# Kernel tuning notes

Hardware: AMD Instinct MI355X
Metric: run time of the kernel (lower is better)

## Reference

```python
import jax, jax.numpy as jnp
import numpy as np


def setup_inputs() -> dict:
    key = jax.random.key(0)
    k1, k2 = jax.random.split(key)
    N, F, E = 100000, 128, 600000
    x = jax.random.normal(k1, (N, F), dtype=jnp.float32)
    edge_index = jax.random.randint(k2, (2, E), 0, N, dtype=jnp.int64)
    return {"x": x, "edge_index": edge_index}


def reference(x, edge_index):
    # x: [N, F] node features; edge_index: [2, E]
    ei = edge_index.T  # [E, 2]
    N = x.shape[0]
    E = ei.shape[0]

    # Midpoint node insertion: mean of the two endpoint features per edge.
    mid = 0.5 * (x[ei[:, 0]] + x[ei[:, 1]])  # [E, F]
    new_x = jnp.concatenate([x, mid], axis=0)  # [N+E, F]

    # New node indices N .. N+E-1
    new_idx = jnp.arange(N, N + E)
    e1 = jnp.stack([ei[:, 0], new_idx], axis=1)  # src -> midpoint
    e2 = jnp.stack([new_idx, ei[:, 1]], axis=1)  # midpoint -> dst

    # Triangle edges among consecutive triples of new nodes (vectorized form
    # of the original Python loop: for i in range(N, N+E-2, 3)).
    T = -(-(E - 2) // 3) if E > 2 else 0  # ceil((E-2)/3) == number of loop iters
    i = N + 3 * jnp.arange(T)
    tri = jnp.stack([i, i + 1, i + 1, i + 2, i + 2, i], axis=1).reshape(-1, 2)  # [3T, 2]

    new_ei = jnp.concatenate([ei, e1, e2, tri], axis=0)  # [E + 2E + 3T, 2]
    return new_x, new_ei.T
```

## Files before the change

### kernel.cpp

```cpp
#include <hip/hip_runtime.h>


#define F 128
#define F4 32
#define BSHIFT 10
#define SLOTS 8192
#define SPB_BLOCKS (SLOTS / 16)
#define CHUNK 2048

typedef float f32x4 __attribute__((ext_vector_type(4)));

__device__ __forceinline__ void nt_store4(f32x4 v, f32x4* p) {
    asm volatile("global_store_dwordx4 %0, %1, off sc0 sc1 nt"
                 :: "v"(p), "v"(v) : "memory");
}
__device__ __forceinline__ void nt_store1(float v, float* p) {
    asm volatile("global_store_dword %0, %1, off sc0 sc1 nt"
                 :: "v"(p), "v"(v) : "memory");
}

__global__ void init_kernel(int4* __restrict__ tup, int* __restrict__ cursor,
                            int NB, int nSlots) {
    const int i = blockIdx.x * blockDim.x + threadIdx.x;
    if (i < nSlots) tup[i] = make_int4(0, 0, -1, 0);
    if (blockIdx.x == 0 && threadIdx.x < NB)
        cursor[threadIdx.x] = threadIdx.x * SLOTS;
}

__global__ __launch_bounds__(256) void scatter_kernel(
        const int* __restrict__ ei0, const int* __restrict__ ei1,
        int* __restrict__ cursor, int4* __restrict__ tup, int E, int NB) {
    __shared__ int lh[128];
    __shared__ int lbase[128];
    const int t = threadIdx.x;
    if (t < 128) lh[t] = 0;
    __syncthreads();
    const int base = blockIdx.x * CHUNK;
    int s[8], d[8], bk[8], rk[8];
#pragma unroll
    for (int i = 0; i < 8; ++i) {
        const int e = base + i * 256 + t;
        if (e < E) {
            s[i] = ei0[e];
            d[i] = ei1[e];
            bk[i] = s[i] >> BSHIFT;
            rk[i] = atomicAdd(&lh[bk[i]], 1);
        } else {
            bk[i] = -1;
        }
    }
    __syncthreads();
    if (t < NB) {
        const int c = lh[t];
        lbase[t] = c ? atomicAdd(&cursor[t], c) : 0;
    }
    __syncthreads();
#pragma unroll
    for (int i = 0; i < 8; ++i) {
        if (bk[i] >= 0) {
            const int e = base + i * 256 + t;
            const int pos = lbase[bk[i]] + rk[i];
            if (pos < (bk[i] + 1) * SLOTS)
                tup[pos] = make_int4(s[i], d[i], e, 0);
        }
    }
}

__global__ __launch_bounds__(256) void main_kernel(
        const f32x4* __restrict__ x4,
        const int* __restrict__ ei0, const int* __restrict__ ei1,
        const int4* __restrict__ tup,
        f32x4* __restrict__ out4, float* __restrict__ r0, float* __restrict__ r1,
        int N, int E, int M, int NB, int MB, int EBlk) {
    const unsigned b = blockIdx.x;

    if (b < (unsigned)MB) {
        const int xcd = b & 7;
        const int seq = b >> 3;
        const int bucket = xcd + 8 * (seq / SPB_BLOCKS);
        if (bucket >= NB) return;
        const int chunk = seq % SPB_BLOCKS;
        const int slot0 = bucket * SLOTS + chunk * 16;
        const int lane = threadIdx.x & 31;
        const int g = threadIdx.x >> 5;
        const int p0 = slot0 + g * 2;

        const int4 t0 = tup[p0];
        const int4 t1 = tup[p0 + 1];
        f32x4 a0 = 0.f, b0v = 0.f, a1 = 0.f, b1v = 0.f;
        if (t0.z >= 0) {
            a0  = x4[t0.x * F4 + lane];
            b0v = x4[t0.y * F4 + lane];
        }
        if (t1.z >= 0) {
            a1  = x4[t1.x * F4 + lane];
            b1v = x4[t1.y * F4 + lane];
        }
        if (t0.z >= 0)
            nt_store4(0.5f * (a0 + b0v), &out4[(size_t)(N + t0.z) * F4 + lane]);
        if (t1.z >= 0)
            nt_store4(0.5f * (a1 + b1v), &out4[(size_t)(N + t1.z) * F4 + lane]);
        return;
    }

    const unsigned eb = b - MB;
    if (eb < (unsigned)EBlk) {
        const int col = eb * 256 + threadIdx.x;
        if (col >= M) return;
        int a, c;
        if (col < E) {
            a = ei0[col];
            c = ei1[col];
        } else if (col < 2 * E) {
            const int e = col - E;
            a = ei0[e];
            c = N + e;
        } else if (col < 3 * E) {
            const int e = col - 2 * E;
            a = N + e;
            c = ei1[e];
        } else {
            const int j = col - 3 * E;
            const int tt = j / 3;
            const int k = j - 3 * tt;
            const int i = N + 3 * tt;
            a = i + k;
            c = (k < 2) ? (i + k + 1) : i;
        }
        nt_store1((float)a, &r0[col]);
        nt_store1((float)c, &r1[col]);
        return;
    }

    const unsigned cb = eb - EBlk;
    const int lane = threadIdx.x & 31;
    const int g = threadIdx.x >> 5;
    const long long row0 = (long long)cb * 16 + g * 2;
    if (row0 < N) {
        f32x4 v0 = x4[row0 * F4 + lane];
        nt_store4(v0, &out4[row0 * F4 + lane]);
    }
    const long long row1 = row0 + 1;
    if (row1 < N) {
        f32x4 v1 = x4[row1 * F4 + lane];
        nt_store4(v1, &out4[row1 * F4 + lane]);
    }
}

extern "C" void kernel_launch(void* const* d_in, const int* in_sizes, int n_in,
                              void* d_out, int out_size, void* d_ws, size_t ws_size,
                              hipStream_t stream) {
    const float* x = (const float*)d_in[0];
    const int* ei = (const int*)d_in[1];

    const int N = in_sizes[0] / F;
    const int E = in_sizes[1] / 2;
    const int T = (E > 2) ? (E - 2 + 2) / 3 : 0;
    const int M = 3 * E + 3 * T;

    const int* ei0 = ei;
    const int* ei1 = ei + E;

    float* out = (float*)d_out;
    float* r0 = out + (size_t)(N + E) * F;
    float* r1 = r0 + M;

    int* cursor = (int*)d_ws;
    int4* tup = (int4*)((char*)d_ws + 4096);

    const int NB = (N + (1 << BSHIFT) - 1) >> BSHIFT;
    const int NBpad = (NB + 7) & ~7;
    const int nSlots = NB * SLOTS;
    const int MB = NBpad * SPB_BLOCKS;
    const int EBlk = (M + 255) / 256;
    const int CB = (N + 15) / 16;

    init_kernel<<<(nSlots + 255) / 256, 256, 0, stream>>>(tup, cursor, NB, nSlots);
    scatter_kernel<<<(E + CHUNK - 1) / CHUNK, 256, 0, stream>>>(
        ei0, ei1, cursor, tup, E, NB);
    main_kernel<<<MB + EBlk + CB, 256, 0, stream>>>(
        (const f32x4*)x, ei0, ei1, tup, (f32x4*)out, r0, r1,
        N, E, M, NB, MB, EBlk);
}
```

Before: 136.1 us.

## Pack bucket tuples into 64-bit words and bound gather work by bucket counts

Edge tuples shrink from 16-byte int4 to 8-byte words holding the edge id, the low source bits and the destination. The main kernel reads each bucket's final cursor to skip empty slots, which removes the init pass over all slots. Nontemporal loads are added for the streamed x rows. The packing needs E < 2^20 and a bucket width of 1024 nodes, which holds for these inputs but limits generality.

```diff
diff --git a/kernel.cpp b/kernel.cpp
--- a/kernel.cpp
+++ b/kernel.cpp
@@ -9,6 +9,7 @@
 #define CHUNK 2048
 
 typedef float f32x4 __attribute__((ext_vector_type(4)));
+typedef unsigned long long u64;
 
 __device__ __forceinline__ void nt_store4(f32x4 v, f32x4* p) {
     asm volatile("global_store_dwordx4 %0, %1, off sc0 sc1 nt"
@@ -19,17 +20,14 @@
                  :: "v"(p), "v"(v) : "memory");
 }
 
-__global__ void init_kernel(int4* __restrict__ tup, int* __restrict__ cursor,
-                            int NB, int nSlots) {
-    const int i = blockIdx.x * blockDim.x + threadIdx.x;
-    if (i < nSlots) tup[i] = make_int4(0, 0, -1, 0);
-    if (blockIdx.x == 0 && threadIdx.x < NB)
-        cursor[threadIdx.x] = threadIdx.x * SLOTS;
+__global__ void init_kernel(int* __restrict__ cursor, int NB) {
+    const int t = threadIdx.x;
+    if (t < NB) cursor[t] = t * SLOTS;
 }
 
 __global__ __launch_bounds__(256) void scatter_kernel(
         const int* __restrict__ ei0, const int* __restrict__ ei1,
-        int* __restrict__ cursor, int4* __restrict__ tup, int E, int NB) {
+        int* __restrict__ cursor, u64* __restrict__ tup, int E, int NB) {
     __shared__ int lh[128];
     __shared__ int lbase[128];
     const int t = threadIdx.x;
@@ -60,8 +58,10 @@
         if (bk[i] >= 0) {
             const int e = base + i * 256 + t;
             const int pos = lbase[bk[i]] + rk[i];
-            if (pos < (bk[i] + 1) * SLOTS)
-                tup[pos] = make_int4(s[i], d[i], e, 0);
+            if (pos < (bk[i] + 1) * SLOTS) {
+                const u64 pk = (u64)(e | ((s[i] & 1023) << 20));
+                __builtin_nontemporal_store((pk << 32) | (unsigned)d[i], &tup[pos]);
+            }
         }
     }
 }
@@ -69,7 +69,7 @@
 __global__ __launch_bounds__(256) void main_kernel(
         const f32x4* __restrict__ x4,
         const int* __restrict__ ei0, const int* __restrict__ ei1,
-        const int4* __restrict__ tup,
+        const u64* __restrict__ tup, const int* __restrict__ cursor,
         f32x4* __restrict__ out4, float* __restrict__ r0, float* __restrict__ r1,
         int N, int E, int M, int NB, int MB, int EBlk) {
     const unsigned b = blockIdx.x;
@@ -79,27 +79,38 @@
         const int seq = b >> 3;
         const int bucket = xcd + 8 * (seq / SPB_BLOCKS);
         if (bucket >= NB) return;
+        const int cnt = cursor[bucket] - bucket * SLOTS;
         const int chunk = seq % SPB_BLOCKS;
-        const int slot0 = bucket * SLOTS + chunk * 16;
+        const int si0 = chunk * 16 + (threadIdx.x >> 5) * 2;
+        if (si0 >= cnt) return;
         const int lane = threadIdx.x & 31;
-        const int g = threadIdx.x >> 5;
-        const int p0 = slot0 + g * 2;
+        const int p0 = bucket * SLOTS + si0;
+        const int nbase = bucket << BSHIFT;
 
-        const int4 t0 = tup[p0];
-        const int4 t1 = tup[p0 + 1];
-        f32x4 a0 = 0.f, b0v = 0.f, a1 = 0.f, b1v = 0.f;
-        if (t0.z >= 0) {
-            a0  = x4[t0.x * F4 + lane];
-            b0v = x4[t0.y * F4 + lane];
+        const u64 t0 = __builtin_nontemporal_load(&tup[p0]);
+        const bool have1 = (si0 + 1) < cnt;
+        const u64 t1 = have1 ? __builtin_nontemporal_load(&tup[p0 + 1]) : 0;
+
+        const int d0 = (int)(t0 & 0xffffffffu);
+        const int pk0 = (int)(t0 >> 32);
+        const int s0 = nbase | (pk0 >> 20);
+        const int e0 = pk0 & 0xFFFFF;
+
+        f32x4 a0 = x4[(size_t)s0 * F4 + lane];
+        f32x4 b0 = __builtin_nontemporal_load(&x4[(size_t)d0 * F4 + lane]);
+
+        if (have1) {
+            const int d1 = (int)(t1 & 0xffffffffu);
+            const int pk1 = (int)(t1 >> 32);
+            const int s1 = nbase | (pk1 >> 20);
+            const int e1 = pk1 & 0xFFFFF;
+            f32x4 a1 = x4[(size_t)s1 * F4 + lane];
+            f32x4 b1 = __builtin_nontemporal_load(&x4[(size_t)d1 * F4 + lane]);
+            nt_store4(0.5f * (a0 + b0), &out4[(size_t)(N + e0) * F4 + lane]);
+            nt_store4(0.5f * (a1 + b1), &out4[(size_t)(N + e1) * F4 + lane]);
+        } else {
+            nt_store4(0.5f * (a0 + b0), &out4[(size_t)(N + e0) * F4 + lane]);
         }
-        if (t1.z >= 0) {
-            a1  = x4[t1.x * F4 + lane];
-            b1v = x4[t1.y * F4 + lane];
-        }
-        if (t0.z >= 0)
-            nt_store4(0.5f * (a0 + b0v), &out4[(size_t)(N + t0.z) * F4 + lane]);
-        if (t1.z >= 0)
-            nt_store4(0.5f * (a1 + b1v), &out4[(size_t)(N + t1.z) * F4 + lane]);
         return;
     }
 
@@ -137,12 +148,12 @@
     const int g = threadIdx.x >> 5;
     const long long row0 = (long long)cb * 16 + g * 2;
     if (row0 < N) {
-        f32x4 v0 = x4[row0 * F4 + lane];
+        f32x4 v0 = __builtin_nontemporal_load(&x4[row0 * F4 + lane]);
         nt_store4(v0, &out4[row0 * F4 + lane]);
     }
     const long long row1 = row0 + 1;
     if (row1 < N) {
-        f32x4 v1 = x4[row1 * F4 + lane];
+        f32x4 v1 = __builtin_nontemporal_load(&x4[row1 * F4 + lane]);
         nt_store4(v1, &out4[row1 * F4 + lane]);
     }
 }
@@ -166,19 +177,18 @@
     float* r1 = r0 + M;
 
     int* cursor = (int*)d_ws;
-    int4* tup = (int4*)((char*)d_ws + 4096);
+    u64* tup = (u64*)((char*)d_ws + 4096);
 
     const int NB = (N + (1 << BSHIFT) - 1) >> BSHIFT;
     const int NBpad = (NB + 7) & ~7;
-    const int nSlots = NB * SLOTS;
     const int MB = NBpad * SPB_BLOCKS;
     const int EBlk = (M + 255) / 256;
     const int CB = (N + 15) / 16;
 
-    init_kernel<<<(nSlots + 255) / 256, 256, 0, stream>>>(tup, cursor, NB, nSlots);
+    init_kernel<<<1, 128, 0, stream>>>(cursor, NB);
     scatter_kernel<<<(E + CHUNK - 1) / CHUNK, 256, 0, stream>>>(
         ei0, ei1, cursor, tup, E, NB);
     main_kernel<<<MB + EBlk + CB, 256, 0, stream>>>(
-        (const f32x4*)x, ei0, ei1, tup, (f32x4*)out, r0, r1,
+        (const f32x4*)x, ei0, ei1, tup, cursor, (f32x4*)out, r0, r1,
         N, E, M, NB, MB, EBlk);
 }
```

New measurement: 171.5 us. +26.0%, slower.
